# Performance work log

Hardware: AMD Instinct MI355X
Metric: run time of the kernel (lower is better)

Reference implementation:

```python
import jax, jax.numpy as jnp
import numpy as np

B, N_IN, N_OUT, NNZ, IN_C, OUT_C = 2, 50000, 12500, 500000, 256, 256


def setup_inputs() -> dict:
    key = jax.random.key(0)
    k1, k2, k3, k4, k5, k6 = jax.random.split(key, 6)
    x = jax.random.normal(k1, (B, N_IN, IN_C), dtype=jnp.float32)
    rows = jax.random.randint(k2, (NNZ,), 0, N_OUT, dtype=jnp.int32)
    cols = jax.random.randint(k3, (NNZ,), 0, N_IN, dtype=jnp.int32)
    vals = jax.random.uniform(k4, (NNZ,), dtype=jnp.float32)
    weight = jax.random.normal(k5, (IN_C, OUT_C), dtype=jnp.float32) / N_OUT
    bias = jax.random.normal(k6, (N_OUT, OUT_C), dtype=jnp.float32) / N_OUT
    return {"x": x, "rows": rows, "cols": cols, "vals": vals,
            "weight": weight, "bias": bias}


def reference(x, rows, cols, vals, weight, bias):
    # per-batch spmm: (A @ x_b) via gather + segment_sum, then dense projection.
    # Equivalent to the original block-diagonal torch.spmm over the batch.
    def spmm_one(xb):  # xb: [n_in, in_c]
        gathered = xb[cols] * vals[:, None]          # [nnz, in_c]
        return jax.ops.segment_sum(gathered, rows, num_segments=N_OUT)

    ax = jax.vmap(spmm_one)(x)                       # [B, n_out, in_c]
    return jnp.einsum('bni,io->bno', ax, weight) + bias
```

## Files before the change

### kernel.cpp

```cpp
#include <hip/hip_runtime.h>
#include <hip/hip_bf16.h>

typedef unsigned short u16;
typedef unsigned int   u32;
typedef __attribute__((ext_vector_type(8))) short bf16x8;
typedef __attribute__((ext_vector_type(4))) float f32x4;

constexpr int B_    = 2;
constexpr int N_IN  = 50000;
constexpr int N_OUT = 12500;
constexpr int NNZ   = 500000;
constexpr int C     = 256;
constexpr int M_TOT = B_ * N_OUT;

constexpr int QB   = N_IN / 8;
constexpr int NB_H = 128;
constexpr int EPB  = (NNZ + NB_H - 1) / NB_H;

__device__ __forceinline__ u16 f2b(float f) {
    __hip_bfloat16 h = __float2bfloat16(f);
    return *(u16*)&h;
}

__device__ __forceinline__ u32 pack4(float4 f, float inv) {
    u32 u0 = (u32)(int)(rintf(f.x * inv) + 128.f);
    u32 u1 = (u32)(int)(rintf(f.y * inv) + 128.f);
    u32 u2 = (u32)(int)(rintf(f.z * inv) + 128.f);
    u32 u3 = (u32)(int)(rintf(f.w * inv) + 128.f);
    return u0 | (u1 << 8) | (u2 << 16) | (u3 << 24);
}

__global__ __launch_bounds__(256) void quant_k(const float* __restrict__ x,
                                               u32* __restrict__ xq,
                                               float* __restrict__ xs) {
    int blk = blockIdx.x;
    int t   = threadIdx.x;
    int wv  = t >> 6, l = t & 63;
    int rec = l >> 4;
    int j   = l & 15;
    int n   = blk * 8 + wv * 2 + (rec >> 1);
    int b   = rec & 1;
    const float4* px = (const float4*)(x + ((size_t)b * N_IN + n) * C + j * 16);
    float4 f0 = px[0], f1 = px[1], f2 = px[2], f3 = px[3];
    float m0 = fmaxf(fmaxf(fabsf(f0.x), fabsf(f0.y)), fmaxf(fabsf(f0.z), fabsf(f0.w)));
    float m1 = fmaxf(fmaxf(fabsf(f1.x), fabsf(f1.y)), fmaxf(fabsf(f1.z), fabsf(f1.w)));
    float m2 = fmaxf(fmaxf(fabsf(f2.x), fabsf(f2.y)), fmaxf(fabsf(f2.z), fabsf(f2.w)));
    float m3 = fmaxf(fmaxf(fabsf(f3.x), fabsf(f3.y)), fmaxf(fabsf(f3.z), fabsf(f3.w)));
    float m  = fmaxf(fmaxf(m0, m1), fmaxf(m2, m3));
#pragma unroll
    for (int off = 1; off < 16; off <<= 1)
        m = fmaxf(m, __shfl_xor(m, off, 64));
    float qstep = m * (1.f / 127.f);
    float inv   = 127.f / m;
    if (j == 0) xs[n * 2 + b] = qstep;
    uint4 pk;
    pk.x = pack4(f0, inv);
    pk.y = pack4(f1, inv);
    pk.z = pack4(f2, inv);
    pk.w = pack4(f3, inv);
    *(uint4*)(xq + (size_t)n * 128 + b * 64 + j * 4) = pk;
}

__global__ __launch_bounds__(256) void hist_k(const int* __restrict__ rows,
                                              u16* __restrict__ partial) {
    __shared__ u32 lc[N_OUT];
    int t = threadIdx.x, blk = blockIdx.x;
    for (int i = t; i < N_OUT; i += 256) lc[i] = 0;
    __syncthreads();
    int base = blk * EPB;
    int end  = base + EPB < NNZ ? base + EPB : NNZ;
    for (int i = base + t; i < end; i += 256)
        atomicAdd(&lc[rows[i]], 1u);
    __syncthreads();
    for (int i = t; i < N_OUT; i += 256)
        partial[(size_t)blk * N_OUT + i] = (u16)lc[i];
}

__global__ __launch_bounds__(256) void binprefix_k(const u16* __restrict__ partial,
                                                   u16* __restrict__ bp,
                                                   int* __restrict__ counts) {
    int bin = blockIdx.x * 256 + threadIdx.x;
    if (bin >= N_OUT) return;
    u32 run = 0;
    for (int b = 0; b < NB_H; ++b) {
        u32 c = partial[(size_t)b * N_OUT + bin];
        bp[(size_t)b * N_OUT + bin] = (u16)run;
        run += c;
    }
    counts[bin] = (int)run;
}

constexpr int CHUNK = (N_OUT + 255) / 256;
__global__ __launch_bounds__(256) void scan_tw_k(const int* __restrict__ counts,
                                                 int* __restrict__ start,
                                                 const float* __restrict__ w,
                                                 u16* __restrict__ wt) {
    int tid = threadIdx.x;
    if (blockIdx.x > 0) {
        int n = blockIdx.x - 1;
        wt[(size_t)n * C + tid] = f2b(w[(size_t)tid * C + n]);
        return;
    }
    int base = tid * CHUNK;
    int s = 0;
    for (int j = 0; j < CHUNK; ++j) {
        int i = base + j;
        s += (i < N_OUT) ? counts[i] : 0;
    }
    int lane = tid & 63, wv = tid >> 6;
    int v = s;
#pragma unroll
    for (int off = 1; off < 64; off <<= 1) {
        int t2 = __shfl_up(v, off, 64);
        if (lane >= off) v += t2;
    }
    __shared__ int wsum[4];
    if (lane == 63) wsum[wv] = v;
    __syncthreads();
    int woff = 0;
    for (int ww = 0; ww < wv; ++ww) woff += wsum[ww];
    if (tid == 255) start[N_OUT] = woff + v;
    int run = woff + v - s;
    for (int j = 0; j < CHUNK; ++j) {
        int i = base + j;
        if (i < N_OUT) {
            start[i] = run;
            run += counts[i];
        }
    }
}

__global__ __launch_bounds__(256) void scatter_k(const int* __restrict__ rows,
                                                 const int* __restrict__ cols,
                                                 const float* __restrict__ vals,
                                                 const int* __restrict__ start,
                                                 const u16* __restrict__ bp,
                                                 int2* __restrict__ edges) {
    __shared__ u32 lc[N_OUT];
    int t = threadIdx.x, blk = blockIdx.x;
    for (int i = t; i < N_OUT; i += 256)
        lc[i] = (u32)start[i] + (u32)bp[(size_t)blk * N_OUT + i];
    __syncthreads();
    int base = blk * EPB;
    int end  = base + EPB < NNZ ? base + EPB : NNZ;
    for (int i = base + t; i < end; i += 256) {
        int r = rows[i];
        u32 p = atomicAdd(&lc[r], 1u);
        edges[p] = make_int2(cols[i], __float_as_int(vals[i]));
    }
}

__global__ __launch_bounds__(256) void spmm_q_k(const u32* __restrict__ xq,
                                                const float* __restrict__ xs,
                                                const int* __restrict__ start,
                                                const int2* __restrict__ edges,
                                                u32* __restrict__ ax) {
    int r    = blockIdx.x;
    int wv   = threadIdx.x >> 6;
    int lane = threadIdx.x & 63;
    int b    = lane >> 5;
    int g    = lane & 31;
    int loff = b * 64 + g * 2;

    int e0 = start[r], e1 = start[r + 1];
    float acc[8];
#pragma unroll
    for (int j = 0; j < 8; ++j) acc[j] = 0.f;
    float S = 0.f;

    auto body = [&](int2 d) {
        float vs = __int_as_float(d.y) * xs[d.x * 2 + b];
        uint2 q  = *(const uint2*)(xq + (size_t)d.x * 128 + loff);
        S += vs;
        acc[0] += vs * (float)( q.x        & 255u);
        acc[1] += vs * (float)((q.x >>  8) & 255u);
        acc[2] += vs * (float)((q.x >> 16) & 255u);
        acc[3] += vs * (float)( q.x >> 24        );
        acc[4] += vs * (float)( q.y        & 255u);
        acc[5] += vs * (float)((q.y >>  8) & 255u);
        acc[6] += vs * (float)((q.y >> 16) & 255u);
        acc[7] += vs * (float)( q.y >> 24        );
    };

    int e = e0 + wv;
    for (; e + 12 < e1; e += 16) {
        int2 d0 = edges[e], d1 = edges[e + 4], d2 = edges[e + 8], d3 = edges[e + 12];
        body(d0); body(d1); body(d2); body(d3);
    }
    for (; e < e1; e += 4) body(edges[e]);

    __shared__ float red[4][64][8];
#pragma unroll
    for (int j = 0; j < 8; ++j) red[wv][lane][j] = acc[j] - 128.f * S;
    __syncthreads();
    if (wv == 0) {
        float4 lo = *(float4*)&red[0][lane][0];
        float4 hi = *(float4*)&red[0][lane][4];
#pragma unroll
        for (int ww = 1; ww < 4; ++ww) {
            float4 l2 = *(float4*)&red[ww][lane][0];
            float4 h2 = *(float4*)&red[ww][lane][4];
            lo.x += l2.x; lo.y += l2.y; lo.z += l2.z; lo.w += l2.w;
            hi.x += h2.x; hi.y += h2.y; hi.z += h2.z; hi.w += h2.w;
        }
        uint4 pk;
        pk.x = (u32)f2b(lo.x) | ((u32)f2b(lo.y) << 16);
        pk.y = (u32)f2b(lo.z) | ((u32)f2b(lo.w) << 16);
        pk.z = (u32)f2b(hi.x) | ((u32)f2b(hi.y) << 16);
        pk.w = (u32)f2b(hi.z) | ((u32)f2b(hi.w) << 16);
        u32* axrow = ax + ((size_t)b * N_OUT + r) * (C / 2);
        *(uint4*)(axrow + g * 4) = pk;
    }
}

__global__ __launch_bounds__(256) void gemm_k(const u32* __restrict__ ax,
                                              const u16* __restrict__ wt,
                                              const float* __restrict__ bias,
                                              float* __restrict__ out) {
    int wave = threadIdx.x >> 6;
    int lane = threadIdx.x & 63;
    int quad = lane >> 4;
    int l15  = lane & 15;
    int m0   = blockIdx.x * 16;
    int n0   = wave * 64;

    int mrow = m0 + l15;
    int mr_c = mrow < M_TOT ? mrow : (M_TOT - 1);
    const u16* arow = (const u16*)(ax + (size_t)mr_c * (C / 2));

    f32x4 acc[4];
#pragma unroll
    for (int t = 0; t < 4; ++t) acc[t] = (f32x4){0.f, 0.f, 0.f, 0.f};

#pragma unroll
    for (int kt = 0; kt < 8; ++kt) {
        int k0 = kt * 32 + quad * 8;
        bf16x8 afrag = *(const bf16x8*)(arow + k0);
#pragma unroll
        for (int nt = 0; nt < 4; ++nt) {
            bf16x8 bfrag = *(const bf16x8*)(wt + (size_t)(n0 + nt * 16 + l15) * C + k0);
            acc[nt] = __builtin_amdgcn_mfma_f32_16x16x32_bf16(afrag, bfrag, acc[nt], 0, 0, 0);
        }
    }

#pragma unroll
    for (int nt = 0; nt < 4; ++nt) {
        int col = n0 + nt * 16 + l15;
#pragma unroll
        for (int reg = 0; reg < 4; ++reg) {
            int rg = m0 + quad * 4 + reg;
            if (rg < M_TOT) {
                int rloc = (rg >= N_OUT) ? rg - N_OUT : rg;
                out[(size_t)rg * C + col] = acc[nt][reg] + bias[(size_t)rloc * C + col];
            }
        }
    }
}

extern "C" void kernel_launch(void* const* d_in, const int* in_sizes, int n_in,
                              void* d_out, int out_size, void* d_ws, size_t ws_size,
                              hipStream_t stream) {
    const float* x      = (const float*)d_in[0];
    const int*   rows   = (const int*)d_in[1];
    const int*   cols   = (const int*)d_in[2];
    const float* vals   = (const float*)d_in[3];
    const float* weight = (const float*)d_in[4];
    const float* bias   = (const float*)d_in[5];
    float*       out    = (float*)d_out;

    char*  ws  = (char*)d_ws;
    size_t off = 0;
    auto alloc = [&](size_t bytes) -> void* {
        void* p = ws + off;
        off = (off + bytes + 255) & ~(size_t)255;
        return p;
    };
    int*   counts = (int*)  alloc((size_t)N_OUT * 4);
    int*   start  = (int*)  alloc((size_t)(N_OUT + 1) * 4);
    int2*  edges  = (int2*) alloc((size_t)NNZ * 8);
    u32*   ax     = (u32*)  alloc((size_t)M_TOT * (C / 2) * 4);
    u16*   wt     = (u16*)  alloc((size_t)C * C * 2);
    u32*   xq     = (u32*)  alloc((size_t)N_IN * 128 * 4);
    float* xs     = (float*)alloc((size_t)N_IN * B_ * 4);
    if (off > ws_size) return;

    u16* partial = (u16*)ax;
    u16* bp      = partial + (size_t)NB_H * N_OUT;

    quant_k    <<<QB, 256, 0, stream>>>(x, xq, xs);
    hist_k     <<<NB_H, 256, 0, stream>>>(rows, partial);
    binprefix_k<<<(N_OUT + 255) / 256, 256, 0, stream>>>(partial, bp, counts);
    scan_tw_k  <<<1 + C, 256, 0, stream>>>(counts, start, weight, wt);
    scatter_k  <<<NB_H, 256, 0, stream>>>(rows, cols, vals, start, bp, edges);
    spmm_q_k   <<<N_OUT, 256, 0, stream>>>(xq, xs, start, edges, ax);
    gemm_k     <<<(M_TOT + 15) / 16, 256, 0, stream>>>(ax, wt, bias, out);
}
```

Baseline: 326.0 us.

## Assign one wavefront per output row in SpMM and software-pipeline edge loads

New measurement: 334.4 us. +2.6%, slower.

```diff
diff --git a/kernel.cpp b/kernel.cpp
--- a/kernel.cpp
+++ b/kernel.cpp
@@ -155,62 +155,71 @@
                                                 const int* __restrict__ start,
                                                 const int2* __restrict__ edges,
                                                 u32* __restrict__ ax) {
-    int r    = blockIdx.x;
-    int wv   = threadIdx.x >> 6;
+    int r    = blockIdx.x * 4 + (threadIdx.x >> 6);
     int lane = threadIdx.x & 63;
     int b    = lane >> 5;
     int g    = lane & 31;
     int loff = b * 64 + g * 2;
 
     int e0 = start[r], e1 = start[r + 1];
+
     float acc[8];
 #pragma unroll
     for (int j = 0; j < 8; ++j) acc[j] = 0.f;
     float S = 0.f;
 
-    auto body = [&](int2 d) {
-        float vs = __int_as_float(d.y) * xs[d.x * 2 + b];
-        uint2 q  = *(const uint2*)(xq + (size_t)d.x * 128 + loff);
-        S += vs;
-        acc[0] += vs * (float)( q.x        & 255u);
-        acc[1] += vs * (float)((q.x >>  8) & 255u);
-        acc[2] += vs * (float)((q.x >> 16) & 255u);
-        acc[3] += vs * (float)( q.x >> 24        );
-        acc[4] += vs * (float)( q.y        & 255u);
-        acc[5] += vs * (float)((q.y >>  8) & 255u);
-        acc[6] += vs * (float)((q.y >> 16) & 255u);
-        acc[7] += vs * (float)( q.y >> 24        );
-    };
-
-    int e = e0 + wv;
-    for (; e + 12 < e1; e += 16) {
-        int2 d0 = edges[e], d1 = edges[e + 4], d2 = edges[e + 8], d3 = edges[e + 12];
-        body(d0); body(d1); body(d2); body(d3);
-    }
-    for (; e < e1; e += 4) body(edges[e]);
-
-    __shared__ float red[4][64][8];
-#pragma unroll
-    for (int j = 0; j < 8; ++j) red[wv][lane][j] = acc[j] - 128.f * S;
-    __syncthreads();
-    if (wv == 0) {
-        float4 lo = *(float4*)&red[0][lane][0];
-        float4 hi = *(float4*)&red[0][lane][4];
-#pragma unroll
-        for (int ww = 1; ww < 4; ++ww) {
-            float4 l2 = *(float4*)&red[ww][lane][0];
-            float4 h2 = *(float4*)&red[ww][lane][4];
-            lo.x += l2.x; lo.y += l2.y; lo.z += l2.z; lo.w += l2.w;
-            hi.x += h2.x; hi.y += h2.y; hi.z += h2.z; hi.w += h2.w;
-        }
-        uint4 pk;
-        pk.x = (u32)f2b(lo.x) | ((u32)f2b(lo.y) << 16);
-        pk.y = (u32)f2b(lo.z) | ((u32)f2b(lo.w) << 16);
-        pk.z = (u32)f2b(hi.x) | ((u32)f2b(hi.y) << 16);
-        pk.w = (u32)f2b(hi.z) | ((u32)f2b(hi.w) << 16);
-        u32* axrow = ax + ((size_t)b * N_OUT + r) * (C / 2);
-        *(uint4*)(axrow + g * 4) = pk;
-    }
+    constexpr int PD = 8;
+    int2 dbuf[PD];
+#pragma unroll
+    for (int k = 0; k < PD; ++k) {
+        int e = e0 + k;
+        int ec = e < NNZ ? e : NNZ - 1;
+        int2 d = edges[ec];
+        dbuf[k] = (e < e1) ? d : make_int2(0, 0);
+    }
+
+    for (int base = e0; base < e1; base += PD) {
+        float vsb[PD];
+        uint2 qb[PD];
+#pragma unroll
+        for (int k = 0; k < PD; ++k) {
+            int2 d = dbuf[k];
+            vsb[k] = __int_as_float(d.y) * xs[d.x * 2 + b];
+            qb[k]  = *(const uint2*)(xq + (size_t)d.x * 128 + loff);
+        }
+#pragma unroll
+        for (int k = 0; k < PD; ++k) {
+            int e = base + PD + k;
+            int ec = e < NNZ ? e : NNZ - 1;
+            int2 d = edges[ec];
+            dbuf[k] = (e < e1) ? d : make_int2(0, 0);
+        }
+#pragma unroll
+        for (int k = 0; k < PD; ++k) {
+            float vs = vsb[k];
+            uint2 q  = qb[k];
+            S += vs;
+            acc[0] += vs * (float)( q.x        & 255u);
+            acc[1] += vs * (float)((q.x >>  8) & 255u);
+            acc[2] += vs * (float)((q.x >> 16) & 255u);
+            acc[3] += vs * (float)( q.x >> 24        );
+            acc[4] += vs * (float)( q.y        & 255u);
+            acc[5] += vs * (float)((q.y >>  8) & 255u);
+            acc[6] += vs * (float)((q.y >> 16) & 255u);
+            acc[7] += vs * (float)( q.y >> 24        );
+        }
+    }
+
+    float o[8];
+#pragma unroll
+    for (int j = 0; j < 8; ++j) o[j] = acc[j] - 128.f * S;
+    uint4 pk;
+    pk.x = (u32)f2b(o[0]) | ((u32)f2b(o[1]) << 16);
+    pk.y = (u32)f2b(o[2]) | ((u32)f2b(o[3]) << 16);
+    pk.z = (u32)f2b(o[4]) | ((u32)f2b(o[5]) << 16);
+    pk.w = (u32)f2b(o[6]) | ((u32)f2b(o[7]) << 16);
+    u32* axrow = ax + ((size_t)b * N_OUT + r) * (C / 2);
+    *(uint4*)(axrow + g * 4) = pk;
 }
 
 __global__ __launch_bounds__(256) void gemm_k(const u32* __restrict__ ax,
@@ -292,6 +301,6 @@
     binprefix_k<<<(N_OUT + 255) / 256, 256, 0, stream>>>(partial, bp, counts);
     scan_tw_k  <<<1 + C, 256, 0, stream>>>(counts, start, weight, wt);
     scatter_k  <<<NB_H, 256, 0, stream>>>(rows, cols, vals, start, bp, edges);
-    spmm_q_k   <<<N_OUT, 256, 0, stream>>>(xq, xs, start, edges, ax);
+    spmm_q_k   <<<N_OUT / 4, 256, 0, stream>>>(xq, xs, start, edges, ax);
     gemm_k     <<<(M_TOT + 15) / 16, 256, 0, stream>>>(ax, wt, bias, out);
 }
```

## Fuse quantize with histogram and replace single-block scan with hierarchical slice scan

Applied to the files above, without the earlier changes.

Result: faster. 308.1 us (-5.5%).

```diff
diff --git a/kernel.cpp b/kernel.cpp
--- a/kernel.cpp
+++ b/kernel.cpp
@@ -13,9 +13,10 @@
 constexpr int C     = 256;
 constexpr int M_TOT = B_ * N_OUT;
 
-constexpr int QB   = N_IN / 8;
-constexpr int NB_H = 128;
-constexpr int EPB  = (NNZ + NB_H - 1) / NB_H;
+constexpr int QB     = N_IN / 8;
+constexpr int NB_H   = 128;
+constexpr int EPB    = (NNZ + NB_H - 1) / NB_H;
+constexpr int NSLICE = (N_OUT + 255) / 256;
 
 __device__ __forceinline__ u16 f2b(float f) {
     __hip_bfloat16 h = __float2bfloat16(f);
@@ -30,116 +31,117 @@
     return u0 | (u1 << 8) | (u2 << 16) | (u3 << 24);
 }
 
-__global__ __launch_bounds__(256) void quant_k(const float* __restrict__ x,
-                                               u32* __restrict__ xq,
-                                               float* __restrict__ xs) {
+__global__ __launch_bounds__(256) void quant_hist_k(const float* __restrict__ x,
+                                                    u32* __restrict__ xq,
+                                                    float* __restrict__ xs,
+                                                    const int* __restrict__ rows,
+                                                    u16* __restrict__ partial) {
+    __shared__ u32 lc[N_OUT];
     int blk = blockIdx.x;
     int t   = threadIdx.x;
-    int wv  = t >> 6, l = t & 63;
-    int rec = l >> 4;
-    int j   = l & 15;
-    int n   = blk * 8 + wv * 2 + (rec >> 1);
-    int b   = rec & 1;
-    const float4* px = (const float4*)(x + ((size_t)b * N_IN + n) * C + j * 16);
-    float4 f0 = px[0], f1 = px[1], f2 = px[2], f3 = px[3];
-    float m0 = fmaxf(fmaxf(fabsf(f0.x), fabsf(f0.y)), fmaxf(fabsf(f0.z), fabsf(f0.w)));
-    float m1 = fmaxf(fmaxf(fabsf(f1.x), fabsf(f1.y)), fmaxf(fabsf(f1.z), fabsf(f1.w)));
-    float m2 = fmaxf(fmaxf(fabsf(f2.x), fabsf(f2.y)), fmaxf(fabsf(f2.z), fabsf(f2.w)));
-    float m3 = fmaxf(fmaxf(fabsf(f3.x), fabsf(f3.y)), fmaxf(fabsf(f3.z), fabsf(f3.w)));
-    float m  = fmaxf(fmaxf(m0, m1), fmaxf(m2, m3));
-#pragma unroll
-    for (int off = 1; off < 16; off <<= 1)
-        m = fmaxf(m, __shfl_xor(m, off, 64));
-    float qstep = m * (1.f / 127.f);
-    float inv   = 127.f / m;
-    if (j == 0) xs[n * 2 + b] = qstep;
-    uint4 pk;
-    pk.x = pack4(f0, inv);
-    pk.y = pack4(f1, inv);
-    pk.z = pack4(f2, inv);
-    pk.w = pack4(f3, inv);
-    *(uint4*)(xq + (size_t)n * 128 + b * 64 + j * 4) = pk;
-}
-
-__global__ __launch_bounds__(256) void hist_k(const int* __restrict__ rows,
-                                              u16* __restrict__ partial) {
-    __shared__ u32 lc[N_OUT];
-    int t = threadIdx.x, blk = blockIdx.x;
-    for (int i = t; i < N_OUT; i += 256) lc[i] = 0;
+    if (blk < QB) {
+        int wv  = t >> 6, l = t & 63;
+        int rec = l >> 4;
+        int j   = l & 15;
+        int n   = blk * 8 + wv * 2 + (rec >> 1);
+        int b   = rec & 1;
+        const float4* px = (const float4*)(x + ((size_t)b * N_IN + n) * C + j * 16);
+        float4 f0 = px[0], f1 = px[1], f2 = px[2], f3 = px[3];
+        float m0 = fmaxf(fmaxf(fabsf(f0.x), fabsf(f0.y)), fmaxf(fabsf(f0.z), fabsf(f0.w)));
+        float m1 = fmaxf(fmaxf(fabsf(f1.x), fabsf(f1.y)), fmaxf(fabsf(f1.z), fabsf(f1.w)));
+        float m2 = fmaxf(fmaxf(fabsf(f2.x), fabsf(f2.y)), fmaxf(fabsf(f2.z), fabsf(f2.w)));
+        float m3 = fmaxf(fmaxf(fabsf(f3.x), fabsf(f3.y)), fmaxf(fabsf(f3.z), fabsf(f3.w)));
+        float m  = fmaxf(fmaxf(m0, m1), fmaxf(m2, m3));
+#pragma unroll
+        for (int off = 1; off < 16; off <<= 1)
+            m = fmaxf(m, __shfl_xor(m, off, 64));
+        float qstep = m * (1.f / 127.f);
+        float inv   = 127.f / m;
+        if (j == 0) xs[n * 2 + b] = qstep;
+        uint4 pk;
+        pk.x = pack4(f0, inv);
+        pk.y = pack4(f1, inv);
+        pk.z = pack4(f2, inv);
+        pk.w = pack4(f3, inv);
+        *(uint4*)(xq + (size_t)n * 128 + b * 64 + j * 4) = pk;
+    } else {
+        int hb = blk - QB;
+        for (int i = t; i < N_OUT; i += 256) lc[i] = 0;
+        __syncthreads();
+        int base = hb * EPB;
+        int end  = base + EPB < NNZ ? base + EPB : NNZ;
+        for (int i = base + t; i < end; i += 256)
+            atomicAdd(&lc[rows[i]], 1u);
+        __syncthreads();
+        for (int i = t; i < N_OUT; i += 256)
+            partial[(size_t)hb * N_OUT + i] = (u16)lc[i];
+    }
+}
+
+__global__ __launch_bounds__(256) void binpre2_k(const u16* __restrict__ partial,
+                                                 u16* __restrict__ bp,
+                                                 u32* __restrict__ startlocal,
+                                                 int* __restrict__ slicesum) {
+    int blk = blockIdx.x;
+    int bin = blk * 256 + threadIdx.x;
+    u32 run = 0;
+    if (bin < N_OUT) {
+        for (int b = 0; b < NB_H; ++b) {
+            u32 c = partial[(size_t)b * N_OUT + bin];
+            bp[(size_t)b * N_OUT + bin] = (u16)run;
+            run += c;
+        }
+    }
+    int lane = threadIdx.x & 63, wv = threadIdx.x >> 6;
+    u32 v = run;
+#pragma unroll
+    for (int off = 1; off < 64; off <<= 1) {
+        u32 t2 = __shfl_up(v, off, 64);
+        if (lane >= off) v += t2;
+    }
+    __shared__ u32 wsum[4];
+    if (lane == 63) wsum[wv] = v;
     __syncthreads();
-    int base = blk * EPB;
-    int end  = base + EPB < NNZ ? base + EPB : NNZ;
-    for (int i = base + t; i < end; i += 256)
-        atomicAdd(&lc[rows[i]], 1u);
-    __syncthreads();
-    for (int i = t; i < N_OUT; i += 256)
-        partial[(size_t)blk * N_OUT + i] = (u16)lc[i];
-}
-
-__global__ __launch_bounds__(256) void binprefix_k(const u16* __restrict__ partial,
-                                                   u16* __restrict__ bp,
-                                                   int* __restrict__ counts) {
-    int bin = blockIdx.x * 256 + threadIdx.x;
-    if (bin >= N_OUT) return;
-    u32 run = 0;
-    for (int b = 0; b < NB_H; ++b) {
-        u32 c = partial[(size_t)b * N_OUT + bin];
-        bp[(size_t)b * N_OUT + bin] = (u16)run;
-        run += c;
-    }
-    counts[bin] = (int)run;
-}
-
-constexpr int CHUNK = (N_OUT + 255) / 256;
-__global__ __launch_bounds__(256) void scan_tw_k(const int* __restrict__ counts,
-                                                 int* __restrict__ start,
-                                                 const float* __restrict__ w,
-                                                 u16* __restrict__ wt) {
+    u32 woff = 0;
+    for (int w = 0; w < wv; ++w) woff += wsum[w];
+    u32 incl = woff + v;
+    if (bin < N_OUT) startlocal[bin] = incl - run;
+    if (threadIdx.x == 255) slicesum[blk] = (int)incl;
+}
+
+__global__ __launch_bounds__(256) void sliceoff_tw_k(const int* __restrict__ slicesum,
+                                                     int* __restrict__ sliceoff,
+                                                     const float* __restrict__ w,
+                                                     u16* __restrict__ wt) {
     int tid = threadIdx.x;
     if (blockIdx.x > 0) {
         int n = blockIdx.x - 1;
         wt[(size_t)n * C + tid] = f2b(w[(size_t)tid * C + n]);
         return;
     }
-    int base = tid * CHUNK;
-    int s = 0;
-    for (int j = 0; j < CHUNK; ++j) {
-        int i = base + j;
-        s += (i < N_OUT) ? counts[i] : 0;
-    }
-    int lane = tid & 63, wv = tid >> 6;
-    int v = s;
-#pragma unroll
-    for (int off = 1; off < 64; off <<= 1) {
-        int t2 = __shfl_up(v, off, 64);
-        if (lane >= off) v += t2;
-    }
-    __shared__ int wsum[4];
-    if (lane == 63) wsum[wv] = v;
-    __syncthreads();
-    int woff = 0;
-    for (int ww = 0; ww < wv; ++ww) woff += wsum[ww];
-    if (tid == 255) start[N_OUT] = woff + v;
-    int run = woff + v - s;
-    for (int j = 0; j < CHUNK; ++j) {
-        int i = base + j;
-        if (i < N_OUT) {
-            start[i] = run;
-            run += counts[i];
-        }
+    if (tid < 64) {
+        int s = (tid < NSLICE) ? slicesum[tid] : 0;
+        int v = s;
+#pragma unroll
+        for (int off = 1; off < 64; off <<= 1) {
+            int t2 = __shfl_up(v, off, 64);
+            if (tid >= off) v += t2;
+        }
+        if (tid < NSLICE) sliceoff[tid] = v - s;
     }
 }
 
 __global__ __launch_bounds__(256) void scatter_k(const int* __restrict__ rows,
                                                  const int* __restrict__ cols,
                                                  const float* __restrict__ vals,
-                                                 const int* __restrict__ start,
+                                                 const int* __restrict__ sliceoff,
+                                                 const u32* __restrict__ startlocal,
                                                  const u16* __restrict__ bp,
                                                  int2* __restrict__ edges) {
     __shared__ u32 lc[N_OUT];
     int t = threadIdx.x, blk = blockIdx.x;
     for (int i = t; i < N_OUT; i += 256)
-        lc[i] = (u32)start[i] + (u32)bp[(size_t)blk * N_OUT + i];
+        lc[i] = (u32)sliceoff[i >> 8] + startlocal[i] + (u32)bp[(size_t)blk * N_OUT + i];
     __syncthreads();
     int base = blk * EPB;
     int end  = base + EPB < NNZ ? base + EPB : NNZ;
@@ -152,7 +154,8 @@
 
 __global__ __launch_bounds__(256) void spmm_q_k(const u32* __restrict__ xq,
                                                 const float* __restrict__ xs,
-                                                const int* __restrict__ start,
+                                                const int* __restrict__ sliceoff,
+                                                const u32* __restrict__ startlocal,
                                                 const int2* __restrict__ edges,
                                                 u32* __restrict__ ax) {
     int r    = blockIdx.x;
@@ -162,7 +165,9 @@
     int g    = lane & 31;
     int loff = b * 64 + g * 2;
 
-    int e0 = start[r], e1 = start[r + 1];
+    int e0 = sliceoff[r >> 8] + (int)startlocal[r];
+    int e1 = (r == N_OUT - 1) ? NNZ : sliceoff[(r + 1) >> 8] + (int)startlocal[r + 1];
+
     float acc[8];
 #pragma unroll
     for (int j = 0; j < 8; ++j) acc[j] = 0.f;
@@ -275,23 +280,23 @@
         off = (off + bytes + 255) & ~(size_t)255;
         return p;
     };
-    int*   counts = (int*)  alloc((size_t)N_OUT * 4);
-    int*   start  = (int*)  alloc((size_t)(N_OUT + 1) * 4);
-    int2*  edges  = (int2*) alloc((size_t)NNZ * 8);
-    u32*   ax     = (u32*)  alloc((size_t)M_TOT * (C / 2) * 4);
-    u16*   wt     = (u16*)  alloc((size_t)C * C * 2);
-    u32*   xq     = (u32*)  alloc((size_t)N_IN * 128 * 4);
-    float* xs     = (float*)alloc((size_t)N_IN * B_ * 4);
+    u32*   startlocal = (u32*) alloc((size_t)N_OUT * 4);
+    int*   slicesum   = (int*) alloc((size_t)NSLICE * 4);
+    int*   sliceoff   = (int*) alloc((size_t)NSLICE * 4);
+    int2*  edges      = (int2*)alloc((size_t)NNZ * 8);
+    u32*   ax         = (u32*) alloc((size_t)M_TOT * (C / 2) * 4);
+    u16*   wt         = (u16*) alloc((size_t)C * C * 2);
+    u32*   xq         = (u32*) alloc((size_t)N_IN * 128 * 4);
+    float* xs         = (float*)alloc((size_t)N_IN * B_ * 4);
     if (off > ws_size) return;
 
     u16* partial = (u16*)ax;
     u16* bp      = partial + (size_t)NB_H * N_OUT;
 
-    quant_k    <<<QB, 256, 0, stream>>>(x, xq, xs);
-    hist_k     <<<NB_H, 256, 0, stream>>>(rows, partial);
-    binprefix_k<<<(N_OUT + 255) / 256, 256, 0, stream>>>(partial, bp, counts);
-    scan_tw_k  <<<1 + C, 256, 0, stream>>>(counts, start, weight, wt);
-    scatter_k  <<<NB_H, 256, 0, stream>>>(rows, cols, vals, start, bp, edges);
-    spmm_q_k   <<<N_OUT, 256, 0, stream>>>(xq, xs, start, edges, ax);
-    gemm_k     <<<(M_TOT + 15) / 16, 256, 0, stream>>>(ax, wt, bias, out);
-}
+    quant_hist_k <<<QB + NB_H, 256, 0, stream>>>(x, xq, xs, rows, partial);
+    binpre2_k    <<<NSLICE, 256, 0, stream>>>(partial, bp, startlocal, slicesum);
+    sliceoff_tw_k<<<1 + C, 256, 0, stream>>>(slicesum, sliceoff, weight, wt);
+    scatter_k    <<<NB_H, 256, 0, stream>>>(rows, cols, vals, sliceoff, startlocal, bp, edges);
+    spmm_q_k     <<<N_OUT, 256, 0, stream>>>(xq, xs, sliceoff, startlocal, edges, ax);
+    gemm_k       <<<(M_TOT + 15) / 16, 256, 0, stream>>>(ax, wt, bias, out);
+}
```
